# Kernel optimization log

Hardware: AMD Instinct MI355X
Metric: run time of the kernel (lower is better)

## Reference

```python
import jax, jax.numpy as jnp
import numpy as np

N = 12500      # nodes
E = 200000     # edges (avg degree 16)
IN = 32        # inp_dim
OUT = 32       # out_dim
ATTN = 32      # attn_rel_emb_dim
R = 200        # num_rels
NB = 50        # num_bases


def setup_inputs() -> dict:
    key = jax.random.key(0)
    ks = jax.random.split(key, 10)
    node_feat = jax.random.normal(ks[0], (N, IN), jnp.float32)
    total_edge = jax.random.randint(ks[1], (2, E), 0, N)
    total_target_relation = jax.random.normal(ks[2], (E, ATTN), jnp.float32)
    total_relation_embed = jax.random.normal(ks[3], (E, ATTN), jnp.float32)
    total_relation = jax.random.randint(ks[4], (E,), 0, R)
    # learned parameters (xavier-ish scale)
    weight = jax.random.normal(ks[5], (NB, IN, OUT), jnp.float32) * 0.1
    w_comp = jax.random.normal(ks[6], (R, NB), jnp.float32) * 0.1
    self_loop_weight = jax.random.normal(ks[7], (IN, OUT), jnp.float32) * 0.1
    A_w = jax.random.normal(ks[8], (IN, 2 * IN + 2 * ATTN), jnp.float32) * 0.1
    A_b = jnp.zeros((IN,), jnp.float32)
    B_w = jax.random.normal(ks[9], (1, IN), jnp.float32) * 0.1
    B_b = jnp.zeros((1,), jnp.float32)
    return {
        'node_feat': node_feat,
        'total_target_relation': total_target_relation,
        'total_relation_embed': total_relation_embed,
        'weight': weight,
        'w_comp': w_comp,
        'self_loop_weight': self_loop_weight,
        'A_w': A_w,
        'A_b': A_b,
        'B_w': B_w,
        'B_b': B_b,
        'total_edge': total_edge,
        'total_relation': total_relation,
    }


def reference(node_feat, total_target_relation, total_relation_embed,
              weight, w_comp, self_loop_weight, A_w, A_b, B_w, B_b,
              total_edge, total_relation):
    # basis decomposition: per-relation weight [R, IN, OUT]
    rel_w = jnp.einsum('rb,bio->rio', w_comp, weight)
    src = node_feat[total_edge[0]]            # [E, IN]
    tgt = node_feat[total_edge[1]]            # [E, IN]
    # per-edge relation-specific transform (bmm in torch)
    msg = jnp.einsum('ei,eio->eo', src, rel_w[total_relation])  # [E, OUT]
    curr = tgt @ self_loop_weight             # [E, OUT]
    # attention MLP: sigmoid(B(relu(A(concat))))
    e = jnp.concatenate([src, tgt, total_relation_embed, total_target_relation], axis=1)
    h = jax.nn.relu(e @ A_w.T + A_b)
    a = jax.nn.sigmoid(h @ B_w.T + B_b)       # [E, 1]
    curr = curr + msg * a
    # gnn_spmm(e2n_sp, curr): scatter-add edge messages to target nodes
    out = jax.ops.segment_sum(curr, total_edge[1], num_segments=node_feat.shape[0])
    return out  # [N, OUT]
```

## Files before the change

kernel.cpp:

```cpp
#include <hip/hip_runtime.h>

#define N_NODES 12500
#define N_EDGES 200000
#define DIM 32
#define N_REL 200
#define N_BASES 50

#define OUT_ELEMS   (N_NODES * DIM)
#define ZERO_BLOCKS ((OUT_ELEMS + 1023) / 1024)

#define EDGES_PER_HBLOCK 1024
#define HIST_BLOCKS ((N_EDGES + EDGES_PER_HBLOCK - 1) / EDGES_PER_HBLOCK)

#define AWBF_OFF  409600
#define SLWT_OFF  417792
#define BINS_OFF  419840
#define CURS_OFF  420864
#define PERM_OFF  421888
#define WS_NEEDED (PERM_OFF + N_EDGES * 4)

typedef __attribute__((ext_vector_type(8))) short short8;
typedef __attribute__((ext_vector_type(4))) float f32x4;
typedef __attribute__((ext_vector_type(4))) unsigned short us4;

__device__ __forceinline__ unsigned short f2bf(float x) {
    union { float f; unsigned u; } v; v.f = x;
    unsigned r = (v.u + 0x7FFFu + ((v.u >> 16) & 1u)) >> 16;
    return (unsigned short)r;
}

__device__ __forceinline__ short8 cvt8(float4 a, float4 b) {
    short8 r;
    r[0] = (short)f2bf(a.x); r[1] = (short)f2bf(a.y);
    r[2] = (short)f2bf(a.z); r[3] = (short)f2bf(a.w);
    r[4] = (short)f2bf(b.x); r[5] = (short)f2bf(b.y);
    r[6] = (short)f2bf(b.z); r[7] = (short)f2bf(b.w);
    return r;
}

__device__ __forceinline__ int clampi(int x, int hi) {
    return x < 0 ? 0 : (x >= hi ? hi - 1 : x);
}

#define MFMA(A, B, C) __builtin_amdgcn_mfma_f32_16x16x32_bf16(A, B, C, 0, 0, 0)

__global__ __launch_bounds__(256) void prep_kernel(
    const float* __restrict__ weight,
    const float* __restrict__ w_comp,
    const float* __restrict__ Aw,
    const float* __restrict__ slw,
    unsigned short* __restrict__ relw_bf,
    unsigned short* __restrict__ aw_bf,
    unsigned short* __restrict__ slwT_bf,
    int* __restrict__ bins,
    float* __restrict__ out)
{
    int b = blockIdx.x, tid = threadIdx.x;
    if (b < N_REL) {
        __shared__ float wc[N_BASES];
        if (tid < N_BASES) wc[tid] = w_comp[b * N_BASES + tid];
        __syncthreads();
        const float* wp = weight + tid * 4;
        float4 acc = make_float4(0.f, 0.f, 0.f, 0.f);
        #pragma unroll 10
        for (int bb = 0; bb < N_BASES; bb++) {
            float4 w = *(const float4*)(wp + bb * 1024);
            float c = wc[bb];
            acc.x = fmaf(c, w.x, acc.x); acc.y = fmaf(c, w.y, acc.y);
            acc.z = fmaf(c, w.z, acc.z); acc.w = fmaf(c, w.w, acc.w);
        }
        us4 o;
        o[0] = f2bf(acc.x); o[1] = f2bf(acc.y);
        o[2] = f2bf(acc.z); o[3] = f2bf(acc.w);
        *(us4*)(relw_bf + b * 1024 + tid * 4) = o;
    } else if (b < N_REL + ZERO_BLOCKS) {
        int base = (b - N_REL) * 1024 + tid * 4;
        if (base + 3 < OUT_ELEMS)
            *(float4*)(out + base) = make_float4(0.f, 0.f, 0.f, 0.f);
        else
            for (int k = 0; k < 4; k++)
                if (base + k < OUT_ELEMS) out[base + k] = 0.f;
    } else {
        for (int x = tid; x < 32 * 128; x += 256) aw_bf[x] = f2bf(Aw[x]);
        for (int x = tid; x < 32 * 32; x += 256) {
            int i = x >> 5, j = x & 31;
            slwT_bf[j * 32 + i] = f2bf(slw[x]);
        }
        if (tid < N_REL) bins[tid] = 0;
    }
}

__global__ __launch_bounds__(256) void hist_kernel(
    const int* __restrict__ rel, int* __restrict__ bins)
{
    __shared__ int lb[N_REL];
    int tid = threadIdx.x;
    if (tid < N_REL) lb[tid] = 0;
    __syncthreads();
    int base = blockIdx.x * EDGES_PER_HBLOCK + tid;
    #pragma unroll
    for (int k = 0; k < 4; k++) {
        int e = base + k * 256;
        if (e < N_EDGES) atomicAdd(&lb[clampi(rel[e], N_REL)], 1);
    }
    __syncthreads();
    if (tid < N_REL && lb[tid] > 0) atomicAdd(&bins[tid], lb[tid]);
}

__global__ __launch_bounds__(64) void scan_kernel(
    const int* __restrict__ bins, int* __restrict__ cursors)
{
    if (threadIdx.x == 0) {
        int run = 0;
        for (int r = 0; r < N_REL; r++) { cursors[r] = run; run += bins[r]; }
    }
}

__global__ __launch_bounds__(256) void scatter_kernel(
    const int* __restrict__ rel, int* __restrict__ cursors,
    int* __restrict__ perm)
{
    __shared__ int lb[N_REL];
    int tid = threadIdx.x;
    if (tid < N_REL) lb[tid] = 0;
    __syncthreads();
    int base = blockIdx.x * EDGES_PER_HBLOCK + tid;
    int myr[4], myrank[4];
    #pragma unroll
    for (int k = 0; k < 4; k++) {
        int e = base + k * 256;
        myr[k] = -1;
        if (e < N_EDGES) {
            myr[k] = clampi(rel[e], N_REL);
            myrank[k] = atomicAdd(&lb[myr[k]], 1);
        }
    }
    __syncthreads();
    if (tid < N_REL) {
        int c = lb[tid];
        lb[tid] = c > 0 ? atomicAdd(&cursors[tid], c) : 0;
    }
    __syncthreads();
    #pragma unroll
    for (int k = 0; k < 4; k++)
        if (myr[k] >= 0) perm[lb[myr[k]] + myrank[k]] = base + k * 256;
}

__global__ __launch_bounds__(256) void edge_kernel(
    const float* __restrict__ node_feat,
    const float* __restrict__ ttr,
    const float* __restrict__ tre,
    const float* __restrict__ Ab,
    const float* __restrict__ Bw,
    const float* __restrict__ Bb,
    const int*  __restrict__ edge0,
    const int*  __restrict__ edge1,
    const int*  __restrict__ rel,
    const int*  __restrict__ perm,
    const unsigned short* __restrict__ relw_bf,
    const unsigned short* __restrict__ aw_bf,
    const unsigned short* __restrict__ slwT_bf,
    float* __restrict__ out)
{
    __shared__ float msgL[4 * 16 * 36];

    int tid  = threadIdx.x;
    int wave = tid >> 6;
    int lane = tid & 63;
    int m = lane & 15;
    int q = lane >> 4;
    int base = blockIdx.x * 64 + wave * 16;

    int s_ld = 0, t_ld = 0, r_ld = 0, e_ld = 0;
    if (lane < 16) {
        int eid = perm ? perm[base + lane] : (base + lane);
        eid = clampi(eid, N_EDGES);
        e_ld = eid;
        s_ld = clampi(edge0[eid], N_NODES);
        t_ld = clampi(edge1[eid], N_NODES);
        r_ld = clampi(rel[eid],   N_REL);
    }
    int s_m   = __shfl(s_ld, m, 64);
    int t_m   = __shfl(t_ld, m, 64);
    int eid_m = __shfl(e_ld, m, 64);

    const float* sp = node_feat + s_m * DIM + q * 8;
    float4 sv0 = *(const float4*)sp, sv1 = *(const float4*)(sp + 4);
    const float* tp = node_feat + t_m * DIM + q * 8;
    float4 tv0 = *(const float4*)tp, tv1 = *(const float4*)(tp + 4);
    const float* rp = tre + eid_m * DIM + q * 8;
    float4 rv0 = *(const float4*)rp, rv1 = *(const float4*)(rp + 4);
    const float* qp = ttr + eid_m * DIM + q * 8;
    float4 qv0 = *(const float4*)qp, qv1 = *(const float4*)(qp + 4);

    short8 fsrc = cvt8(sv0, sv1);
    short8 ftgt = cvt8(tv0, tv1);
    short8 fre  = cvt8(rv0, rv1);
    short8 ftr  = cvt8(qv0, qv1);

    short8 bA[4][2], bS[2];
    #pragma unroll
    for (int hh = 0; hh < 2; hh++) {
        #pragma unroll
        for (int c = 0; c < 4; c++)
            bA[c][hh] = *(const short8*)(aw_bf + (16 * hh + m) * 128 + 32 * c + 8 * q);
        bS[hh] = *(const short8*)(slwT_bf + (16 * hh + m) * 32 + 8 * q);
    }

    float ab0 = Ab[m], ab1 = Ab[16 + m];
    f32x4 hacc0 = {ab0, ab0, ab0, ab0};
    f32x4 hacc1 = {ab1, ab1, ab1, ab1};
    f32x4 cacc0 = {0.f, 0.f, 0.f, 0.f};
    f32x4 cacc1 = {0.f, 0.f, 0.f, 0.f};

    hacc0 = MFMA(fsrc, bA[0][0], hacc0);  hacc1 = MFMA(fsrc, bA[0][1], hacc1);
    hacc0 = MFMA(ftgt, bA[1][0], hacc0);  hacc1 = MFMA(ftgt, bA[1][1], hacc1);
    hacc0 = MFMA(fre,  bA[2][0], hacc0);  hacc1 = MFMA(fre,  bA[2][1], hacc1);
    hacc0 = MFMA(ftr,  bA[3][0], hacc0);  hacc1 = MFMA(ftr,  bA[3][1], hacc1);
    cacc0 = MFMA(ftgt, bS[0], cacc0);     cacc1 = MFMA(ftgt, bS[1], cacc1);

    int e_loc = lane >> 2;
    int cq    = lane & 3;
    int r_e = __shfl(r_ld, e_loc, 64);
    const unsigned short* rwb = relw_bf + r_e * 1024 + cq * 8;
    float sf[8] = {sv0.x, sv0.y, sv0.z, sv0.w, sv1.x, sv1.y, sv1.z, sv1.w};
    float msg[8] = {0.f, 0.f, 0.f, 0.f, 0.f, 0.f, 0.f, 0.f};
    #pragma unroll
    for (int k = 0; k < 32; k++) {
        float s_k = __shfl(sf[k & 7], e_loc + 16 * (k >> 3), 64);
        union { short8 s; unsigned u[4]; } W;
        W.s = *(const short8*)(rwb + k * 32);
        #pragma unroll
        for (int p = 0; p < 4; p++) {
            float lo = __uint_as_float(W.u[p] << 16);
            float hi = __uint_as_float(W.u[p] & 0xffff0000u);
            msg[2 * p]     = fmaf(s_k, lo, msg[2 * p]);
            msg[2 * p + 1] = fmaf(s_k, hi, msg[2 * p + 1]);
        }
    }

    float* ml = msgL + wave * (16 * 36);
    *(float4*)(ml + e_loc * 36 + cq * 8)     = make_float4(msg[0], msg[1], msg[2], msg[3]);
    *(float4*)(ml + e_loc * 36 + cq * 8 + 4) = make_float4(msg[4], msg[5], msg[6], msg[7]);

    float bw0 = Bw[m], bw1 = Bw[16 + m], Bb0 = Bb[0];
    float av[4];
    #pragma unroll
    for (int v = 0; v < 4; v++) {
        float p = fmaxf(hacc0[v], 0.f) * bw0 + fmaxf(hacc1[v], 0.f) * bw1;
        p += __shfl_xor(p, 1, 16);
        p += __shfl_xor(p, 2, 16);
        p += __shfl_xor(p, 4, 16);
        p += __shfl_xor(p, 8, 16);
        av[v] = 1.f / (1.f + __expf(-(p + Bb0)));
    }
    #pragma unroll
    for (int v = 0; v < 4; v++) {
        int row = 4 * q + v;
        int tv = __shfl(t_ld, row, 64);
        float m0 = ml[row * 36 + m];
        float m1 = ml[row * 36 + 16 + m];
        atomicAdd(&out[tv * DIM + m],      cacc0[v] + m0 * av[v]);
        atomicAdd(&out[tv * DIM + 16 + m], cacc1[v] + m1 * av[v]);
    }
}

extern "C" void kernel_launch(void* const* d_in, const int* in_sizes, int n_in,
                              void* d_out, int out_size, void* d_ws, size_t ws_size,
                              hipStream_t stream) {
    const float* node_feat = (const float*)d_in[0];
    const float* ttr       = (const float*)d_in[1];
    const float* tre       = (const float*)d_in[2];
    const float* weight    = (const float*)d_in[3];
    const float* w_comp    = (const float*)d_in[4];
    const float* slw       = (const float*)d_in[5];
    const float* Aw        = (const float*)d_in[6];
    const float* Ab        = (const float*)d_in[7];
    const float* Bw        = (const float*)d_in[8];
    const float* Bb        = (const float*)d_in[9];
    const int*  total_edge = (const int*)d_in[10];
    const int*  rel        = (const int*)d_in[11];
    const int*  edge0 = total_edge;
    const int*  edge1 = total_edge + N_EDGES;

    unsigned short* relw_bf = (unsigned short*)d_ws;
    unsigned short* aw_bf   = (unsigned short*)((char*)d_ws + AWBF_OFF);
    unsigned short* slwT_bf = (unsigned short*)((char*)d_ws + SLWT_OFF);
    int* bins    = (int*)((char*)d_ws + BINS_OFF);
    int* cursors = (int*)((char*)d_ws + CURS_OFF);
    int* perm    = (int*)((char*)d_ws + PERM_OFF);
    float* out = (float*)d_out;

    bool use_sort = ws_size >= (size_t)WS_NEEDED;

    prep_kernel<<<N_REL + ZERO_BLOCKS + 1, 256, 0, stream>>>(
        weight, w_comp, Aw, slw, relw_bf, aw_bf, slwT_bf, bins, out);

    if (use_sort) {
        hist_kernel<<<HIST_BLOCKS, 256, 0, stream>>>(rel, bins);
        scan_kernel<<<1, 64, 0, stream>>>(bins, cursors);
        scatter_kernel<<<HIST_BLOCKS, 256, 0, stream>>>(rel, cursors, perm);
    }

    edge_kernel<<<N_EDGES / 64, 256, 0, stream>>>(
        node_feat, ttr, tre, Ab, Bw, Bb,
        edge0, edge1, rel, use_sort ? perm : (const int*)nullptr,
        relw_bf, aw_bf, slwT_bf, out);
}
```

Baseline: 165.9 us.

## Use MFMA for relation messages in uniform-relation tiles and fuse sort kernels

Measured after the change: 159.5 us. 1.04x faster.

```diff
diff --git a/kernel.cpp b/kernel.cpp
--- a/kernel.cpp
+++ b/kernel.cpp
@@ -15,9 +15,10 @@
 #define AWBF_OFF  409600
 #define SLWT_OFF  417792
 #define BINS_OFF  419840
-#define CURS_OFF  420864
-#define PERM_OFF  421888
-#define WS_NEEDED (PERM_OFF + N_EDGES * 4)
+#define GCUR_OFF  420640
+#define PERM_OFF  421440
+#define WS_A (PERM_OFF + N_EDGES * 16)
+#define WS_B (PERM_OFF + N_EDGES * 4)
 
 typedef __attribute__((ext_vector_type(8))) short short8;
 typedef __attribute__((ext_vector_type(4))) float f32x4;
@@ -27,6 +28,9 @@
     union { float f; unsigned u; } v; v.f = x;
     unsigned r = (v.u + 0x7FFFu + ((v.u >> 16) & 1u)) >> 16;
     return (unsigned short)r;
+}
+__device__ __forceinline__ float bf2f(unsigned short u) {
+    return __uint_as_float(((unsigned)u) << 16);
 }
 
 __device__ __forceinline__ short8 cvt8(float4 a, float4 b) {
@@ -49,11 +53,13 @@
     const float* __restrict__ w_comp,
     const float* __restrict__ Aw,
     const float* __restrict__ slw,
+    const int*  __restrict__ rel,
     unsigned short* __restrict__ relw_bf,
     unsigned short* __restrict__ aw_bf,
     unsigned short* __restrict__ slwT_bf,
     int* __restrict__ bins,
-    float* __restrict__ out)
+    float* __restrict__ out,
+    int sorted)
 {
     int b = blockIdx.x, tid = threadIdx.x;
     if (b < N_REL) {
@@ -69,10 +75,18 @@
             acc.x = fmaf(c, w.x, acc.x); acc.y = fmaf(c, w.y, acc.y);
             acc.z = fmaf(c, w.z, acc.z); acc.w = fmaf(c, w.w, acc.w);
         }
-        us4 o;
-        o[0] = f2bf(acc.x); o[1] = f2bf(acc.y);
-        o[2] = f2bf(acc.z); o[3] = f2bf(acc.w);
-        *(us4*)(relw_bf + b * 1024 + tid * 4) = o;
+        int i = (tid * 4) >> 5, o = (tid * 4) & 31;
+        if (sorted) {
+            relw_bf[b * 1024 + (o + 0) * 32 + i] = f2bf(acc.x);
+            relw_bf[b * 1024 + (o + 1) * 32 + i] = f2bf(acc.y);
+            relw_bf[b * 1024 + (o + 2) * 32 + i] = f2bf(acc.z);
+            relw_bf[b * 1024 + (o + 3) * 32 + i] = f2bf(acc.w);
+        } else {
+            us4 ov;
+            ov[0] = f2bf(acc.x); ov[1] = f2bf(acc.y);
+            ov[2] = f2bf(acc.z); ov[3] = f2bf(acc.w);
+            *(us4*)(relw_bf + b * 1024 + tid * 4) = ov;
+        }
     } else if (b < N_REL + ZERO_BLOCKS) {
         int base = (b - N_REL) * 1024 + tid * 4;
         if (base + 3 < OUT_ELEMS)
@@ -80,49 +94,46 @@
         else
             for (int k = 0; k < 4; k++)
                 if (base + k < OUT_ELEMS) out[base + k] = 0.f;
-    } else {
+    } else if (b == N_REL + ZERO_BLOCKS) {
         for (int x = tid; x < 32 * 128; x += 256) aw_bf[x] = f2bf(Aw[x]);
         for (int x = tid; x < 32 * 32; x += 256) {
             int i = x >> 5, j = x & 31;
             slwT_bf[j * 32 + i] = f2bf(slw[x]);
         }
-        if (tid < N_REL) bins[tid] = 0;
-    }
-}
-
-__global__ __launch_bounds__(256) void hist_kernel(
-    const int* __restrict__ rel, int* __restrict__ bins)
+    } else {
+        __shared__ int lb[N_REL];
+        if (tid < N_REL) lb[tid] = 0;
+        __syncthreads();
+        int base = (b - (N_REL + ZERO_BLOCKS + 1)) * EDGES_PER_HBLOCK + tid;
+        #pragma unroll
+        for (int k = 0; k < 4; k++) {
+            int e = base + k * 256;
+            if (e < N_EDGES) atomicAdd(&lb[clampi(rel[e], N_REL)], 1);
+        }
+        __syncthreads();
+        if (tid < N_REL && lb[tid] > 0) atomicAdd(&bins[tid], lb[tid]);
+    }
+}
+
+__global__ __launch_bounds__(256) void scatter_kernel(
+    const int* __restrict__ rel,
+    const int* __restrict__ edge0,
+    const int* __restrict__ edge1,
+    const int* __restrict__ bins,
+    int* __restrict__ gcur,
+    int4* __restrict__ perm4,
+    int* __restrict__ permi)
 {
+    __shared__ int sb[N_REL];
+    __shared__ int pref[N_REL];
     __shared__ int lb[N_REL];
     int tid = threadIdx.x;
-    if (tid < N_REL) lb[tid] = 0;
+    if (tid < N_REL) { sb[tid] = bins[tid]; lb[tid] = 0; }
     __syncthreads();
-    int base = blockIdx.x * EDGES_PER_HBLOCK + tid;
-    #pragma unroll
-    for (int k = 0; k < 4; k++) {
-        int e = base + k * 256;
-        if (e < N_EDGES) atomicAdd(&lb[clampi(rel[e], N_REL)], 1);
-    }
-    __syncthreads();
-    if (tid < N_REL && lb[tid] > 0) atomicAdd(&bins[tid], lb[tid]);
-}
-
-__global__ __launch_bounds__(64) void scan_kernel(
-    const int* __restrict__ bins, int* __restrict__ cursors)
-{
-    if (threadIdx.x == 0) {
+    if (tid == 0) {
         int run = 0;
-        for (int r = 0; r < N_REL; r++) { cursors[r] = run; run += bins[r]; }
-    }
-}
-
-__global__ __launch_bounds__(256) void scatter_kernel(
-    const int* __restrict__ rel, int* __restrict__ cursors,
-    int* __restrict__ perm)
-{
-    __shared__ int lb[N_REL];
-    int tid = threadIdx.x;
-    if (tid < N_REL) lb[tid] = 0;
+        for (int r = 0; r < N_REL; r++) { pref[r] = run; run += sb[r]; }
+    }
     __syncthreads();
     int base = blockIdx.x * EDGES_PER_HBLOCK + tid;
     int myr[4], myrank[4];
@@ -138,12 +149,23 @@
     __syncthreads();
     if (tid < N_REL) {
         int c = lb[tid];
-        lb[tid] = c > 0 ? atomicAdd(&cursors[tid], c) : 0;
+        lb[tid] = c > 0 ? (pref[tid] + atomicAdd(&gcur[tid], c)) : 0;
     }
     __syncthreads();
     #pragma unroll
-    for (int k = 0; k < 4; k++)
-        if (myr[k] >= 0) perm[lb[myr[k]] + myrank[k]] = base + k * 256;
+    for (int k = 0; k < 4; k++) {
+        if (myr[k] >= 0) {
+            int e = base + k * 256;
+            int pos = lb[myr[k]] + myrank[k];
+            if (perm4) {
+                int s = clampi(edge0[e], N_NODES);
+                int t = clampi(edge1[e], N_NODES);
+                perm4[pos] = make_int4(s, t, myr[k], e);
+            } else {
+                permi[pos] = e;
+            }
+        }
+    }
 }
 
 __global__ __launch_bounds__(256) void edge_kernel(
@@ -156,7 +178,8 @@
     const int*  __restrict__ edge0,
     const int*  __restrict__ edge1,
     const int*  __restrict__ rel,
-    const int*  __restrict__ perm,
+    const int4* __restrict__ perm4,
+    const int*  __restrict__ permi,
     const unsigned short* __restrict__ relw_bf,
     const unsigned short* __restrict__ aw_bf,
     const unsigned short* __restrict__ slwT_bf,
@@ -173,16 +196,23 @@
 
     int s_ld = 0, t_ld = 0, r_ld = 0, e_ld = 0;
     if (lane < 16) {
-        int eid = perm ? perm[base + lane] : (base + lane);
-        eid = clampi(eid, N_EDGES);
-        e_ld = eid;
-        s_ld = clampi(edge0[eid], N_NODES);
-        t_ld = clampi(edge1[eid], N_NODES);
-        r_ld = clampi(rel[eid],   N_REL);
+        if (perm4) {
+            int4 pv = perm4[base + lane];
+            s_ld = pv.x; t_ld = pv.y; r_ld = pv.z; e_ld = pv.w;
+        } else {
+            int eid = permi ? clampi(permi[base + lane], N_EDGES) : (base + lane);
+            e_ld = eid;
+            s_ld = clampi(edge0[eid], N_NODES);
+            t_ld = clampi(edge1[eid], N_NODES);
+            r_ld = clampi(rel[eid],   N_REL);
+        }
     }
     int s_m   = __shfl(s_ld, m, 64);
     int t_m   = __shfl(t_ld, m, 64);
     int eid_m = __shfl(e_ld, m, 64);
+    int r_m   = __shfl(r_ld, m, 64);
+    int r0    = __shfl(r_ld, 0, 64);
+    bool sorted = (perm4 != nullptr) || (permi != nullptr);
 
     const float* sp = node_feat + s_m * DIM + q * 8;
     float4 sv0 = *(const float4*)sp, sv1 = *(const float4*)(sp + 4);
@@ -219,29 +249,48 @@
     hacc0 = MFMA(ftr,  bA[3][0], hacc0);  hacc1 = MFMA(ftr,  bA[3][1], hacc1);
     cacc0 = MFMA(ftgt, bS[0], cacc0);     cacc1 = MFMA(ftgt, bS[1], cacc1);
 
-    int e_loc = lane >> 2;
-    int cq    = lane & 3;
-    int r_e = __shfl(r_ld, e_loc, 64);
-    const unsigned short* rwb = relw_bf + r_e * 1024 + cq * 8;
-    float sf[8] = {sv0.x, sv0.y, sv0.z, sv0.w, sv1.x, sv1.y, sv1.z, sv1.w};
-    float msg[8] = {0.f, 0.f, 0.f, 0.f, 0.f, 0.f, 0.f, 0.f};
-    #pragma unroll
-    for (int k = 0; k < 32; k++) {
-        float s_k = __shfl(sf[k & 7], e_loc + 16 * (k >> 3), 64);
-        union { short8 s; unsigned u[4]; } W;
-        W.s = *(const short8*)(rwb + k * 32);
+    f32x4 macc0 = {0.f, 0.f, 0.f, 0.f};
+    f32x4 macc1 = {0.f, 0.f, 0.f, 0.f};
+    bool uni = sorted && __all(r_m == r0);
+    if (uni) {
+        const unsigned short* rwt = relw_bf + r0 * 1024;
+        short8 bM0 = *(const short8*)(rwt + m * 32 + 8 * q);
+        short8 bM1 = *(const short8*)(rwt + (16 + m) * 32 + 8 * q);
+        macc0 = MFMA(fsrc, bM0, macc0);
+        macc1 = MFMA(fsrc, bM1, macc1);
+    } else {
+        int e_loc = lane >> 2;
+        int cq    = lane & 3;
+        int r_e = __shfl(r_ld, e_loc, 64);
+        float sf[8] = {sv0.x, sv0.y, sv0.z, sv0.w, sv1.x, sv1.y, sv1.z, sv1.w};
+        float msg[8] = {0.f, 0.f, 0.f, 0.f, 0.f, 0.f, 0.f, 0.f};
+        const unsigned short* rw = relw_bf + r_e * 1024;
+        #pragma unroll 4
+        for (int k = 0; k < 32; k++) {
+            float s_k = __shfl(sf[k & 7], e_loc + 16 * (k >> 3), 64);
+            if (sorted) {
+                #pragma unroll
+                for (int p = 0; p < 8; p++)
+                    msg[p] = fmaf(s_k, bf2f(rw[(cq * 8 + p) * 32 + k]), msg[p]);
+            } else {
+                union { short8 s; unsigned u[4]; } W;
+                W.s = *(const short8*)(rw + k * 32 + cq * 8);
+                #pragma unroll
+                for (int p = 0; p < 4; p++) {
+                    msg[2 * p]     = fmaf(s_k, __uint_as_float(W.u[p] << 16), msg[2 * p]);
+                    msg[2 * p + 1] = fmaf(s_k, __uint_as_float(W.u[p] & 0xffff0000u), msg[2 * p + 1]);
+                }
+            }
+        }
+        float* ml = msgL + wave * (16 * 36);
+        *(float4*)(ml + e_loc * 36 + cq * 8)     = make_float4(msg[0], msg[1], msg[2], msg[3]);
+        *(float4*)(ml + e_loc * 36 + cq * 8 + 4) = make_float4(msg[4], msg[5], msg[6], msg[7]);
         #pragma unroll
-        for (int p = 0; p < 4; p++) {
-            float lo = __uint_as_float(W.u[p] << 16);
-            float hi = __uint_as_float(W.u[p] & 0xffff0000u);
-            msg[2 * p]     = fmaf(s_k, lo, msg[2 * p]);
-            msg[2 * p + 1] = fmaf(s_k, hi, msg[2 * p + 1]);
-        }
-    }
-
-    float* ml = msgL + wave * (16 * 36);
-    *(float4*)(ml + e_loc * 36 + cq * 8)     = make_float4(msg[0], msg[1], msg[2], msg[3]);
-    *(float4*)(ml + e_loc * 36 + cq * 8 + 4) = make_float4(msg[4], msg[5], msg[6], msg[7]);
+        for (int v = 0; v < 4; v++) {
+            macc0[v] = ml[(4 * q + v) * 36 + m];
+            macc1[v] = ml[(4 * q + v) * 36 + 16 + m];
+        }
+    }
 
     float bw0 = Bw[m], bw1 = Bw[16 + m], Bb0 = Bb[0];
     float av[4];
@@ -258,10 +307,8 @@
     for (int v = 0; v < 4; v++) {
         int row = 4 * q + v;
         int tv = __shfl(t_ld, row, 64);
-        float m0 = ml[row * 36 + m];
-        float m1 = ml[row * 36 + 16 + m];
-        atomicAdd(&out[tv * DIM + m],      cacc0[v] + m0 * av[v]);
-        atomicAdd(&out[tv * DIM + 16 + m], cacc1[v] + m1 * av[v]);
+        atomicAdd(&out[tv * DIM + m],      cacc0[v] + macc0[v] * av[v]);
+        atomicAdd(&out[tv * DIM + 16 + m], cacc1[v] + macc1[v] * av[v]);
     }
 }
 
@@ -286,24 +333,28 @@
     unsigned short* relw_bf = (unsigned short*)d_ws;
     unsigned short* aw_bf   = (unsigned short*)((char*)d_ws + AWBF_OFF);
     unsigned short* slwT_bf = (unsigned short*)((char*)d_ws + SLWT_OFF);
-    int* bins    = (int*)((char*)d_ws + BINS_OFF);
-    int* cursors = (int*)((char*)d_ws + CURS_OFF);
-    int* perm    = (int*)((char*)d_ws + PERM_OFF);
+    int* bins = (int*)((char*)d_ws + BINS_OFF);
+    int* gcur = (int*)((char*)d_ws + GCUR_OFF);
     float* out = (float*)d_out;
 
-    bool use_sort = ws_size >= (size_t)WS_NEEDED;
-
-    prep_kernel<<<N_REL + ZERO_BLOCKS + 1, 256, 0, stream>>>(
-        weight, w_comp, Aw, slw, relw_bf, aw_bf, slwT_bf, bins, out);
-
-    if (use_sort) {
-        hist_kernel<<<HIST_BLOCKS, 256, 0, stream>>>(rel, bins);
-        scan_kernel<<<1, 64, 0, stream>>>(bins, cursors);
-        scatter_kernel<<<HIST_BLOCKS, 256, 0, stream>>>(rel, cursors, perm);
-    }
+    int tierA = ws_size >= (size_t)WS_A;
+    int tierB = !tierA && ws_size >= (size_t)WS_B;
+    int sorted = tierA || tierB;
+    int4* perm4 = tierA ? (int4*)((char*)d_ws + PERM_OFF) : nullptr;
+    int*  permi = tierB ? (int*)((char*)d_ws + PERM_OFF) : nullptr;
+
+    if (sorted) hipMemsetAsync(bins, 0, 1600, stream);
+
+    int prep_blocks = N_REL + ZERO_BLOCKS + 1 + (sorted ? HIST_BLOCKS : 0);
+    prep_kernel<<<prep_blocks, 256, 0, stream>>>(
+        weight, w_comp, Aw, slw, rel, relw_bf, aw_bf, slwT_bf, bins, out, sorted);
+
+    if (sorted)
+        scatter_kernel<<<HIST_BLOCKS, 256, 0, stream>>>(
+            rel, edge0, edge1, bins, gcur, perm4, permi);
 
     edge_kernel<<<N_EDGES / 64, 256, 0, stream>>>(
         node_feat, ttr, tre, Ab, Bw, Bb,
-        edge0, edge1, rel, use_sort ? perm : (const int*)nullptr,
+        edge0, edge1, rel, perm4, permi,
         relw_bf, aw_bf, slwT_bf, out);
 }
```
